# Kernel optimization log

Hardware: AMD Instinct MI355X
Metric: run time of the kernel (lower is better)

Reference implementation:

```python
import jax, jax.numpy as jnp
import numpy as np

NUM_FIELDS = 40
EMBED = 64
# pair indices (i<j) matching itertools.combinations order
_I, _J = np.triu_indices(NUM_FIELDS, k=1)
NUM_PAIRS = _I.shape[0]  # 780


def setup_inputs() -> dict:
    key = jax.random.key(0)
    k1, k2 = jax.random.split(key)
    feature_emb = jax.random.normal(k1, (2048, NUM_FIELDS, EMBED), dtype=jnp.float32)
    bound = 1.0 / np.sqrt(EMBED)  # nn.Linear default init range
    W = jax.random.uniform(k2, (NUM_PAIRS, EMBED, EMBED), dtype=jnp.float32,
                           minval=-bound, maxval=bound)
    return {"feature_emb": feature_emb, "W": W}


def reference(feature_emb, W):
    # field_interaction: for pair p=(i,j): (v_i @ W_p^T) * v_j
    idx_i = jnp.asarray(_I)
    idx_j = jnp.asarray(_J)
    vi = feature_emb[:, idx_i, :]  # [B, P, E]
    vj = feature_emb[:, idx_j, :]  # [B, P, E]
    # nn.Linear: y = x @ W^T  -> einsum over input-feature axis e
    out = jnp.einsum('bpe,pfe->bpf', vi, W) * vj  # [B, P, E]
    return out
```

## Files before the change

kernel.cpp:

```cpp
#include <hip/hip_runtime.h>

#define NUM_FIELDS 40
#define NPAIRS     780
#define EMBED      64
#define BATCH      2048
#define BB         128
#define PT         12
#define NBC        (BATCH/BB)
#define NPC        (NPAIRS/PT)
#define NBLK       (NBC*NPC)

#define NW_ELEMS   (NPAIRS*EMBED*EMBED)
#define NE_ELEMS   (BATCH*NUM_FIELDS*EMBED)
#define NW8        (NW_ELEMS/8)
#define NE8        (NE_ELEMS/8)

typedef __attribute__((ext_vector_type(8))) short bf16x8;
typedef __attribute__((ext_vector_type(4))) short short4v;
typedef __attribute__((ext_vector_type(4))) float f32x4;

__device__ __forceinline__ short f2bf(float f) {
    unsigned u = __builtin_bit_cast(unsigned, f);
    u += 0x7FFFu + ((u >> 16) & 1u);
    return (short)(u >> 16);
}
__device__ __forceinline__ float bf2f(short h) {
    return __builtin_bit_cast(float, (unsigned)((unsigned short)h) << 16);
}

__global__ __launch_bounds__(256)
void cvt_all_bf16(const float* __restrict__ W, const float* __restrict__ emb,
                  short* __restrict__ dst) {
    const int total = NW8 + NE8;
    for (int i = blockIdx.x * 256 + threadIdx.x; i < total; i += gridDim.x * 256) {
        const float* src = (i < NW8) ? (W + (size_t)i * 8)
                                     : (emb + ((size_t)(i - NW8)) * 8);
        float4 a = ((const float4*)src)[0];
        float4 b = ((const float4*)src)[1];
        short4v lo, hi;
        lo.x = f2bf(a.x); lo.y = f2bf(a.y); lo.z = f2bf(a.z); lo.w = f2bf(a.w);
        hi.x = f2bf(b.x); hi.y = f2bf(b.y); hi.z = f2bf(b.z); hi.w = f2bf(b.w);
        ((short4v*)dst)[2 * (size_t)i]     = lo;
        ((short4v*)dst)[2 * (size_t)i + 1] = hi;
    }
}

__global__ __launch_bounds__(256, 4)
void bilinear_direct4(const short* __restrict__ Wbf,
                      const short* __restrict__ embbf,
                      float* __restrict__ out) {
    __shared__ __align__(16) float TR[4][2][16][64];

    const int bid  = blockIdx.x;
    const int orig = (bid & 7) * (NBLK / 8) + (bid >> 3);
    const int bc   = orig % NBC;
    const int pc   = orig / NBC;
    const int bblk = bc * BB;
    const int p0   = pc * PT;

    const int t   = threadIdx.x;
    const int w   = t >> 6;
    const int l   = t & 63;
    const int l15 = l & 15;
    const int l4  = l >> 4;
    const int rl  = l >> 4;

    int fi = 0, rem = p0, cnt = NUM_FIELDS - 1;
    while (rem >= cnt) { rem -= cnt; --cnt; ++fi; }
    int fj = fi + 1 + rem;

    const int r0 = bblk + 16 * w + l15;
    const short* erow0 = embbf + (size_t)r0 * NUM_FIELDS * EMBED;
    const short* erow1 = erow0 + (size_t)64 * NUM_FIELDS * EMBED;

    bf16x8 bfr[2][2];
    {
        const short* v0 = erow0 + (size_t)fi * EMBED + l4 * 8;
        const short* v1 = erow1 + (size_t)fi * EMBED + l4 * 8;
        bfr[0][0] = *(const bf16x8*)(v0);
        bfr[0][1] = *(const bf16x8*)(v0 + 32);
        bfr[1][0] = *(const bf16x8*)(v1);
        bfr[1][1] = *(const bf16x8*)(v1 + 32);
    }

    const short* wb = Wbf + (size_t)p0 * (EMBED * EMBED) + l15 * EMBED + l4 * 8;

    #pragma unroll 2
    for (int pi = 0; pi < PT; ++pi) {
        const int p = p0 + pi;
        const short* wp = wb + (size_t)pi * (EMBED * EMBED);

        bf16x8 afr[8];
        #pragma unroll
        for (int nt = 0; nt < 4; ++nt) {
            afr[2 * nt]     = *(const bf16x8*)(wp + nt * 16 * EMBED);
            afr[2 * nt + 1] = *(const bf16x8*)(wp + nt * 16 * EMBED + 32);
        }

        #pragma unroll
        for (int bt = 0; bt < 2; ++bt) {
            const short* vjrow = (bt ? erow1 : erow0) + (size_t)fj * EMBED;

            short4v vjh[4];
            #pragma unroll
            for (int nt = 0; nt < 4; ++nt)
                vjh[nt] = *(const short4v*)(vjrow + nt * 16 + l4 * 4);

            f32x4 acc[4];
            #pragma unroll
            for (int nt = 0; nt < 4; ++nt) {
                acc[nt].x = 0.f; acc[nt].y = 0.f; acc[nt].z = 0.f; acc[nt].w = 0.f;
                acc[nt] = __builtin_amdgcn_mfma_f32_16x16x32_bf16(afr[2 * nt],     bfr[bt][0], acc[nt], 0, 0, 0);
                acc[nt] = __builtin_amdgcn_mfma_f32_16x16x32_bf16(afr[2 * nt + 1], bfr[bt][1], acc[nt], 0, 0, 0);
            }

            float* myrow = &TR[w][bt][l15][0];
            #pragma unroll
            for (int nt = 0; nt < 4; ++nt) {
                const int slot = (nt * 4 + l4) ^ (l15 & 7);
                f32x4 o;
                o.x = acc[nt].x * bf2f(vjh[nt].x);
                o.y = acc[nt].y * bf2f(vjh[nt].y);
                o.z = acc[nt].z * bf2f(vjh[nt].z);
                o.w = acc[nt].w * bf2f(vjh[nt].w);
                *(f32x4*)(myrow + slot * 4) = o;
            }
        }

        #pragma unroll
        for (int bt = 0; bt < 2; ++bt) {
            #pragma unroll
            for (int k = 0; k < 4; ++k) {
                const int row  = 4 * k + rl;
                const int slot = l15 ^ (row & 7);
                f32x4 v = *(const f32x4*)&TR[w][bt][row][slot * 4];
                float* dstp = out +
                    ((size_t)(bblk + bt * 64 + 16 * w + row) * NPAIRS + p) * EMBED
                    + l15 * 4;
                __builtin_nontemporal_store(v, (f32x4*)dstp);
            }
        }

        int fi_n = fi, fj_n = fj + 1;
        if (fj_n == NUM_FIELDS) { fi_n = fi + 1; fj_n = fi_n + 1; }
        if (fi_n != fi) {
            const short* v0 = erow0 + (size_t)fi_n * EMBED + l4 * 8;
            const short* v1 = erow1 + (size_t)fi_n * EMBED + l4 * 8;
            bfr[0][0] = *(const bf16x8*)(v0);
            bfr[0][1] = *(const bf16x8*)(v0 + 32);
            bfr[1][0] = *(const bf16x8*)(v1);
            bfr[1][1] = *(const bf16x8*)(v1 + 32);
        }
        fi = fi_n; fj = fj_n;
    }
}

__global__ __launch_bounds__(256, 4)
void bilinear_mfma2(const float* __restrict__ emb,
                    const float* __restrict__ Wg,
                    float* __restrict__ out) {
    __shared__ __align__(16) short WbS[2][64][8][8];
    __shared__ __align__(16) short VIS[64][8][8];

    const int FBPT = 26;
    const int FNPC = NPAIRS / FBPT;
    const int FNBLK = (BATCH / 64) * FNPC;
    const int bid  = blockIdx.x;
    const int orig = (bid & 7) * (FNBLK / 8) + (bid >> 3);
    const int bc   = orig % (BATCH / 64);
    const int pc   = orig / (BATCH / 64);
    const int bblk = bc * 64;
    const int p0   = pc * FBPT;
    const int t = threadIdx.x;

    int fi = 0, rem = p0, cnt = NUM_FIELDS - 1;
    while (rem >= cnt) { rem -= cnt; --cnt; ++fi; }
    int fj = fi + 1 + rem;

    {
        const float4* Wp = (const float4*)(Wg + (size_t)p0 * EMBED * EMBED);
        #pragma unroll
        for (int k = 0; k < 4; ++k) {
            int n = t + 256 * k;
            int row = n >> 4, e4 = n & 15;
            float4 wv = Wp[n];
            float4 vv = *(const float4*)(emb +
                          ((size_t)(bblk + row) * NUM_FIELDS + fi) * EMBED + e4 * 4);
            int o = e4 >> 1, half = e4 & 1;
            int slot = o ^ (row & 7);
            short4v cw, cv;
            cw.x = f2bf(wv.x); cw.y = f2bf(wv.y); cw.z = f2bf(wv.z); cw.w = f2bf(wv.w);
            cv.x = f2bf(vv.x); cv.y = f2bf(vv.y); cv.z = f2bf(vv.z); cv.w = f2bf(vv.w);
            *(short4v*)&WbS[0][row][slot][half * 4] = cw;
            *(short4v*)&VIS[row][slot][half * 4] = cv;
        }
    }
    __syncthreads();

    const int w = t >> 6, l = t & 63, l15 = l & 15, l4 = l >> 4;
    const size_t bg = (size_t)(bblk + 16 * w + l15);
    const float* vjbase = emb + bg * NUM_FIELDS * EMBED;
    float*       obase  = out + (bg * NPAIRS) * (size_t)EMBED;

    for (int pi = 0; pi < FBPT; ++pi) {
        const int cur = pi & 1, nxt = cur ^ 1;
        const int p   = p0 + pi;
        int fi_n = fi, fj_n = fj + 1;
        if (fj_n == NUM_FIELDS) { fi_n = fi + 1; fj_n = fi_n + 1; }
        const bool havenext  = (pi + 1 < FBPT);
        const bool fi_change = havenext && (fi_n != fi);

        float4 Wpre[4], Vpre[4];
        if (havenext) {
            const float4* Wp = (const float4*)(Wg + (size_t)(p + 1) * EMBED * EMBED);
            #pragma unroll
            for (int k = 0; k < 4; ++k) Wpre[k] = Wp[t + 256 * k];
        }
        if (fi_change) {
            #pragma unroll
            for (int k = 0; k < 4; ++k) {
                int n = t + 256 * k;
                int row = n >> 4, e4 = n & 15;
                Vpre[k] = *(const float4*)(emb +
                            ((size_t)(bblk + row) * NUM_FIELDS + fi_n) * EMBED + e4 * 4);
            }
        }

        const float* vjrow = vjbase + (size_t)fj * EMBED;
        float4 vj4[4];
        #pragma unroll
        for (int nt = 0; nt < 4; ++nt)
            vj4[nt] = *(const float4*)(vjrow + nt * 16 + l4 * 4);

        bf16x8 bfr[2];
        #pragma unroll
        for (int kk = 0; kk < 2; ++kk) {
            int row  = 16 * w + l15;
            int slot = (kk * 4 + l4) ^ (row & 7);
            bfr[kk] = *(const bf16x8*)&VIS[row][slot][0];
        }

        f32x4 acc[4];
        #pragma unroll
        for (int nt = 0; nt < 4; ++nt) {
            acc[nt].x = 0.f; acc[nt].y = 0.f; acc[nt].z = 0.f; acc[nt].w = 0.f;
            #pragma unroll
            for (int kk = 0; kk < 2; ++kk) {
                int row  = 16 * nt + l15;
                int slot = (kk * 4 + l4) ^ (row & 7);
                bf16x8 afr = *(const bf16x8*)&WbS[cur][row][slot][0];
                acc[nt] = __builtin_amdgcn_mfma_f32_16x16x32_bf16(afr, bfr[kk], acc[nt], 0, 0, 0);
            }
        }

        float* orow = obase + (size_t)p * EMBED;
        #pragma unroll
        for (int nt = 0; nt < 4; ++nt) {
            f32x4 o;
            o.x = acc[nt].x * vj4[nt].x;
            o.y = acc[nt].y * vj4[nt].y;
            o.z = acc[nt].z * vj4[nt].z;
            o.w = acc[nt].w * vj4[nt].w;
            __builtin_nontemporal_store(o, (f32x4*)(orow + nt * 16 + l4 * 4));
        }

        if (havenext) {
            #pragma unroll
            for (int k = 0; k < 4; ++k) {
                int n = t + 256 * k;
                int row = n >> 4, e4 = n & 15;
                int o = e4 >> 1, half = e4 & 1;
                int slot = o ^ (row & 7);
                short4v cw;
                cw.x = f2bf(Wpre[k].x); cw.y = f2bf(Wpre[k].y);
                cw.z = f2bf(Wpre[k].z); cw.w = f2bf(Wpre[k].w);
                *(short4v*)&WbS[nxt][row][slot][half * 4] = cw;
            }
        }
        if (fi_change) {
            __syncthreads();
            #pragma unroll
            for (int k = 0; k < 4; ++k) {
                int n = t + 256 * k;
                int row = n >> 4, e4 = n & 15;
                int o = e4 >> 1, half = e4 & 1;
                int slot = o ^ (row & 7);
                short4v cv;
                cv.x = f2bf(Vpre[k].x); cv.y = f2bf(Vpre[k].y);
                cv.z = f2bf(Vpre[k].z); cv.w = f2bf(Vpre[k].w);
                *(short4v*)&VIS[row][slot][half * 4] = cv;
            }
        }

        fi = fi_n; fj = fj_n;
        __syncthreads();
    }
}

extern "C" void kernel_launch(void* const* d_in, const int* in_sizes, int n_in,
                              void* d_out, int out_size, void* d_ws, size_t ws_size,
                              hipStream_t stream) {
    const float* emb = (const float*)d_in[0];
    const float* W   = (const float*)d_in[1];
    float*       out = (float*)d_out;

    const size_t need = (size_t)(NW_ELEMS + NE_ELEMS) * sizeof(short);
    if (ws_size >= need) {
        short* Wbf   = (short*)d_ws;
        short* embbf = Wbf + NW_ELEMS;
        hipLaunchKernelGGL(cvt_all_bf16, dim3(2048), dim3(256), 0, stream, W, emb, Wbf);
        hipLaunchKernelGGL(bilinear_direct4, dim3(NBLK), dim3(256), 0, stream,
                           Wbf, embbf, out);
    } else {
        hipLaunchKernelGGL(bilinear_mfma2, dim3(960), dim3(256), 0, stream, emb, W, out);
    }
}
```

Before: 141.7 us.

## Stage four pairs per row in LDS so stores write contiguous 1KB runs

The main kernel now handles 64 batch rows and 20 pairs per block instead of 128 rows and 12 pairs. Results for four consecutive pairs are staged in LDS per row, so each wave writes 1 KB contiguous segments of the output rather than 256 B pieces. In exchange, each W tile is reused across half as many batch rows, the LDS staging buffer doubles, and the launch-bounds occupancy hint drops from 4 to 2.

```diff
diff --git a/kernel.cpp b/kernel.cpp
--- a/kernel.cpp
+++ b/kernel.cpp
@@ -4,8 +4,9 @@
 #define NPAIRS     780
 #define EMBED      64
 #define BATCH      2048
-#define BB         128
-#define PT         12
+#define BB         64
+#define PT         20
+#define PSLOT      4
 #define NBC        (BATCH/BB)
 #define NPC        (NPAIRS/PT)
 #define NBLK       (NBC*NPC)
@@ -45,11 +46,11 @@
     }
 }
 
-__global__ __launch_bounds__(256, 4)
-void bilinear_direct4(const short* __restrict__ Wbf,
+__global__ __launch_bounds__(256, 2)
+void bilinear_direct5(const short* __restrict__ Wbf,
                       const short* __restrict__ embbf,
                       float* __restrict__ out) {
-    __shared__ __align__(16) float TR[4][2][16][64];
+    __shared__ __align__(16) float TR[4][16][PSLOT][EMBED];
 
     const int bid  = blockIdx.x;
     const int orig = (bid & 7) * (NBLK / 8) + (bid >> 3);
@@ -63,44 +64,38 @@
     const int l   = t & 63;
     const int l15 = l & 15;
     const int l4  = l >> 4;
-    const int rl  = l >> 4;
 
     int fi = 0, rem = p0, cnt = NUM_FIELDS - 1;
     while (rem >= cnt) { rem -= cnt; --cnt; ++fi; }
     int fj = fi + 1 + rem;
 
     const int r0 = bblk + 16 * w + l15;
-    const short* erow0 = embbf + (size_t)r0 * NUM_FIELDS * EMBED;
-    const short* erow1 = erow0 + (size_t)64 * NUM_FIELDS * EMBED;
-
-    bf16x8 bfr[2][2];
+    const short* erow = embbf + (size_t)r0 * NUM_FIELDS * EMBED;
+    const short* vib  = erow + l4 * 8;
+
+    bf16x8 bfr[2];
     {
-        const short* v0 = erow0 + (size_t)fi * EMBED + l4 * 8;
-        const short* v1 = erow1 + (size_t)fi * EMBED + l4 * 8;
-        bfr[0][0] = *(const bf16x8*)(v0);
-        bfr[0][1] = *(const bf16x8*)(v0 + 32);
-        bfr[1][0] = *(const bf16x8*)(v1);
-        bfr[1][1] = *(const bf16x8*)(v1 + 32);
+        const short* v = vib + (size_t)fi * EMBED;
+        bfr[0] = *(const bf16x8*)(v);
+        bfr[1] = *(const bf16x8*)(v + 32);
     }
 
     const short* wb = Wbf + (size_t)p0 * (EMBED * EMBED) + l15 * EMBED + l4 * 8;
 
-    #pragma unroll 2
-    for (int pi = 0; pi < PT; ++pi) {
-        const int p = p0 + pi;
-        const short* wp = wb + (size_t)pi * (EMBED * EMBED);
-
-        bf16x8 afr[8];
-        #pragma unroll
-        for (int nt = 0; nt < 4; ++nt) {
-            afr[2 * nt]     = *(const bf16x8*)(wp + nt * 16 * EMBED);
-            afr[2 * nt + 1] = *(const bf16x8*)(wp + nt * 16 * EMBED + 32);
-        }
-
-        #pragma unroll
-        for (int bt = 0; bt < 2; ++bt) {
-            const short* vjrow = (bt ? erow1 : erow0) + (size_t)fj * EMBED;
-
+    for (int g = 0; g < PT / PSLOT; ++g) {
+        #pragma unroll
+        for (int ps = 0; ps < PSLOT; ++ps) {
+            const int pi = g * PSLOT + ps;
+            const short* wp = wb + (size_t)pi * (EMBED * EMBED);
+
+            bf16x8 afr[8];
+            #pragma unroll
+            for (int nt = 0; nt < 4; ++nt) {
+                afr[2 * nt]     = *(const bf16x8*)(wp + nt * 16 * EMBED);
+                afr[2 * nt + 1] = *(const bf16x8*)(wp + nt * 16 * EMBED + 32);
+            }
+
+            const short* vjrow = erow + (size_t)fj * EMBED;
             short4v vjh[4];
             #pragma unroll
             for (int nt = 0; nt < 4; ++nt)
@@ -110,11 +105,11 @@
             #pragma unroll
             for (int nt = 0; nt < 4; ++nt) {
                 acc[nt].x = 0.f; acc[nt].y = 0.f; acc[nt].z = 0.f; acc[nt].w = 0.f;
-                acc[nt] = __builtin_amdgcn_mfma_f32_16x16x32_bf16(afr[2 * nt],     bfr[bt][0], acc[nt], 0, 0, 0);
-                acc[nt] = __builtin_amdgcn_mfma_f32_16x16x32_bf16(afr[2 * nt + 1], bfr[bt][1], acc[nt], 0, 0, 0);
-            }
-
-            float* myrow = &TR[w][bt][l15][0];
+                acc[nt] = __builtin_amdgcn_mfma_f32_16x16x32_bf16(afr[2 * nt],     bfr[0], acc[nt], 0, 0, 0);
+                acc[nt] = __builtin_amdgcn_mfma_f32_16x16x32_bf16(afr[2 * nt + 1], bfr[1], acc[nt], 0, 0, 0);
+            }
+
+            float* myrow = &TR[w][l15][ps][0];
             #pragma unroll
             for (int nt = 0; nt < 4; ++nt) {
                 const int slot = (nt * 4 + l4) ^ (l15 & 7);
@@ -125,33 +120,27 @@
                 o.w = acc[nt].w * bf2f(vjh[nt].w);
                 *(f32x4*)(myrow + slot * 4) = o;
             }
-        }
-
-        #pragma unroll
-        for (int bt = 0; bt < 2; ++bt) {
-            #pragma unroll
-            for (int k = 0; k < 4; ++k) {
-                const int row  = 4 * k + rl;
-                const int slot = l15 ^ (row & 7);
-                f32x4 v = *(const f32x4*)&TR[w][bt][row][slot * 4];
-                float* dstp = out +
-                    ((size_t)(bblk + bt * 64 + 16 * w + row) * NPAIRS + p) * EMBED
-                    + l15 * 4;
-                __builtin_nontemporal_store(v, (f32x4*)dstp);
-            }
-        }
-
-        int fi_n = fi, fj_n = fj + 1;
-        if (fj_n == NUM_FIELDS) { fi_n = fi + 1; fj_n = fi_n + 1; }
-        if (fi_n != fi) {
-            const short* v0 = erow0 + (size_t)fi_n * EMBED + l4 * 8;
-            const short* v1 = erow1 + (size_t)fi_n * EMBED + l4 * 8;
-            bfr[0][0] = *(const bf16x8*)(v0);
-            bfr[0][1] = *(const bf16x8*)(v0 + 32);
-            bfr[1][0] = *(const bf16x8*)(v1);
-            bfr[1][1] = *(const bf16x8*)(v1 + 32);
-        }
-        fi = fi_n; fj = fj_n;
+
+            int fi_n = fi, fj_n = fj + 1;
+            if (fj_n == NUM_FIELDS) { fi_n = fi + 1; fj_n = fi_n + 1; }
+            if (fi_n != fi) {
+                const short* v = vib + (size_t)fi_n * EMBED;
+                bfr[0] = *(const bf16x8*)(v);
+                bfr[1] = *(const bf16x8*)(v + 32);
+            }
+            fi = fi_n; fj = fj_n;
+        }
+
+        const int pbase = p0 + g * PSLOT;
+        #pragma unroll
+        for (int r = 0; r < 16; ++r) {
+            const int chunk = l15 ^ (r & 7);
+            f32x4 v = *(const f32x4*)&TR[w][r][l4][chunk * 4];
+            float* dstp = out +
+                ((size_t)(bblk + 16 * w + r) * NPAIRS + pbase + l4) * EMBED
+                + l15 * 4;
+            __builtin_nontemporal_store(v, (f32x4*)dstp);
+        }
     }
 }
 
@@ -309,7 +298,7 @@
         short* Wbf   = (short*)d_ws;
         short* embbf = Wbf + NW_ELEMS;
         hipLaunchKernelGGL(cvt_all_bf16, dim3(2048), dim3(256), 0, stream, W, emb, Wbf);
-        hipLaunchKernelGGL(bilinear_direct4, dim3(NBLK), dim3(256), 0, stream,
+        hipLaunchKernelGGL(bilinear_direct5, dim3(NBLK), dim3(256), 0, stream,
                            Wbf, embbf, out);
     } else {
         hipLaunchKernelGGL(bilinear_mfma2, dim3(960), dim3(256), 0, stream, emb, W, out);
```

Result: slower. 168.9 us (+19.2%).
